# Kernel optimization log

Hardware: AMD Instinct MI355X
Metric: run time of the kernel (lower is better)

The kernel has to match this reference:

```python
import jax, jax.numpy as jnp
import numpy as np

S = 8192          # past KV length
H = 4096          # hidden size
NH = 32           # heads
HD = 128          # head dim
INNER = 16384     # MLP inner (4h)
ROT = 64          # rotary dim per 2D-rope half
NUM_LAYERS = 28
LAYER_ID = 0
ALPHA = (2.0 * NUM_LAYERS) ** 0.5
QK_COEFF = float(LAYER_ID + 1)            # query_key_layer_scaling_coeff
COEFF = (128.0 ** 0.5) * QK_COEFF         # math.sqrt(128) * coeff
EPS = 1e-5


def layernorm(x, w, b):
    mu = jnp.mean(x, axis=-1, keepdims=True)
    var = jnp.var(x, axis=-1, keepdims=True)
    return (x - mu) * jax.lax.rsqrt(var + EPS) * w + b


def rotate_half(x):
    # x: [..., 64]; GLM rotate-half at 32
    return jnp.concatenate([-x[..., 32:], x[..., :32]], axis=-1)


def setup_inputs() -> dict:
    key = jax.random.key(0)
    ks = jax.random.split(key, 16)
    # rotary cache (as in the driver script)
    inv_freq = 1.0 / (10000.0 ** (jnp.arange(0, ROT, 2, dtype=jnp.float32) / ROT))  # [32]
    t = jnp.arange(512, dtype=jnp.float32)
    freqs = jnp.einsum('i,j->ij', t, inv_freq)          # [512,32]
    emb = jnp.concatenate([freqs, freqs], axis=-1)      # [512,64]
    w = lambda k, shp: jax.random.normal(k, shp, dtype=jnp.float32) * 0.02
    return {
        'hidden_states': jax.random.normal(ks[0], (1, H), dtype=jnp.float32),
        'past_key': jax.random.normal(ks[1], (S, NH, HD), dtype=jnp.float32),
        'past_value': jax.random.normal(ks[2], (S, NH, HD), dtype=jnp.float32),
        'cos_cached': jnp.cos(emb),
        'sin_cached': jnp.sin(emb),
        'ln1_w': jnp.ones((H,), jnp.float32), 'ln1_b': jnp.zeros((H,), jnp.float32),
        'qkv_w': w(ks[3], (3 * H, H)), 'qkv_b': w(ks[4], (3 * H,)),
        'dense_w': w(ks[5], (H, H)), 'dense_b': w(ks[6], (H,)),
        'ln2_w': jnp.ones((H,), jnp.float32), 'ln2_b': jnp.zeros((H,), jnp.float32),
        'fc1_w': w(ks[7], (INNER, H)), 'fc1_b': w(ks[8], (INNER,)),
        'fc2_w': w(ks[9], (H, INNER)), 'fc2_b': w(ks[10], (H,)),
        'position_ids': jax.random.randint(ks[11], (1, 1), 0, 512),
        'block_position_ids': jax.random.randint(ks[12], (1, 1), 0, 512),
        'attention_mask': jnp.zeros((1, 1, S + 1), dtype=bool),
    }


def reference(hidden_states, past_key, past_value, cos_cached, sin_cached,
              ln1_w, ln1_b, qkv_w, qkv_b, dense_w, dense_b,
              ln2_w, ln2_b, fc1_w, fc1_b, fc2_w, fc2_b,
              position_ids, block_position_ids, attention_mask):
    # rotary lookups: embedding then transpose(0,1) -> [q_len,1,64]
    pos_cos = jnp.transpose(cos_cached[position_ids], (1, 0, 2))
    pos_sin = jnp.transpose(sin_cached[position_ids], (1, 0, 2))
    blk_cos = jnp.transpose(cos_cached[block_position_ids], (1, 0, 2))
    blk_sin = jnp.transpose(sin_cached[block_position_ids], (1, 0, 2))

    residual = layernorm(hidden_states, ln1_w, ln1_b)          # [1, H]
    qkv = residual @ qkv_w.T + qkv_b                           # [1, 3H]
    qkv = qkv.reshape(-1, NH, 3 * HD)                          # [1, 32, 384]
    query, key_new, value_new = jnp.split(qkv, 3, axis=2)      # each [1,32,128]

    q1, q2 = jnp.split(query, 2, axis=2)                       # [1,32,64] each
    k1, k2 = jnp.split(key_new, 2, axis=2)
    q1 = q1 * pos_cos + rotate_half(q1) * pos_sin
    k1 = k1 * pos_cos + rotate_half(k1) * pos_sin
    q2 = q2 * blk_cos + rotate_half(q2) * blk_sin
    k2 = k2 * blk_cos + rotate_half(k2) * blk_sin
    q = jnp.concatenate([q1, q2], axis=-1)                     # [1,32,128]
    k_new = jnp.concatenate([k1, k2], axis=-1)                 # [1,32,128]

    k = jnp.concatenate([past_key, k_new], axis=0)             # [S+1,32,128]
    v = jnp.concatenate([past_value, value_new], axis=0)       # [S+1,32,128]

    # scores: [heads, q=1, S+1]
    scores = jnp.einsum('qhd,khd->hqk', q / COEFF, k)
    scores = jnp.where(attention_mask, jnp.float32(-10000.0), scores)
    scores = scores * QK_COEFF
    probs = jax.nn.softmax(scores, axis=-1)
    ctx = jnp.einsum('hqk,khd->qhd', probs, v).reshape(-1, H)  # [1,4096]

    attn_out = ctx @ dense_w.T + dense_b
    hidden = residual * ALPHA + attn_out

    residual2 = layernorm(hidden, ln2_w, ln2_b)
    mlp = jax.nn.gelu(residual2 @ fc1_w.T + fc1_b, approximate=True)
    mlp = mlp @ fc2_w.T + fc2_b
    out = residual2 * ALPHA + mlp
    return (out, k, v)
```

## Files before the change

kernel.cpp:

```cpp
#include <hip/hip_runtime.h>
#include <math.h>

#define S_PAST 8192
#define S_TOT  8193
#define HID    4096
#define NH     32
#define HD     128
#define INNER  16384
#define CH     16
#define NCH    512
#define ALPHA_ 7.483314773547883f
#define INV_COEFF 0.08838834764831845f
#define EPS_ 1e-5f

__global__ __launch_bounds__(256) void ln_kernel(const float* __restrict__ xin,
                                                 const float* __restrict__ w,
                                                 const float* __restrict__ b,
                                                 float* __restrict__ out) {
    int tid = threadIdx.x;
    float xs[16];
    float s = 0.f, s2 = 0.f;
#pragma unroll
    for (int i = 0; i < 16; ++i) {
        float v = xin[tid + i * 256];
        xs[i] = v; s += v; s2 += v * v;
    }
    for (int off = 32; off; off >>= 1) {
        s  += __shfl_down(s, off, 64);
        s2 += __shfl_down(s2, off, 64);
    }
    __shared__ float rs[4], rs2[4];
    __shared__ float mu_s, ri_s;
    int wid = tid >> 6, lane = tid & 63;
    if (lane == 0) { rs[wid] = s; rs2[wid] = s2; }
    __syncthreads();
    if (tid == 0) {
        float S1 = rs[0] + rs[1] + rs[2] + rs[3];
        float S2 = rs2[0] + rs2[1] + rs2[2] + rs2[3];
        float mu = S1 / HID;
        float var = S2 / HID - mu * mu;
        mu_s = mu;
        ri_s = rsqrtf(var + EPS_);
    }
    __syncthreads();
    float mu = mu_s, ri = ri_s;
#pragma unroll
    for (int i = 0; i < 16; ++i) {
        int idx = tid + i * 256;
        out[idx] = (xs[i] - mu) * ri * w[idx] + b[idx];
    }
}

template <int C, int MODE>
__global__ __launch_bounds__(256) void gemv_kernel(
        const float* __restrict__ Wm, const float* __restrict__ bias,
        const float* __restrict__ x, float* __restrict__ y,
        const float* __restrict__ res) {
    int wid = threadIdx.x >> 6, lane = threadIdx.x & 63;
    int r = blockIdx.x * 4 + wid;
    const float4* __restrict__ rowv = (const float4*)(Wm + (size_t)r * C);
    const float4* __restrict__ xv = (const float4*)x;
    constexpr int IT = C / 4 / 64;
    float acc0 = 0.f, acc1 = 0.f;
#pragma unroll 8
    for (int it = 0; it < IT; it += 2) {
        float4 w0 = rowv[lane + it * 64];
        float4 x0 = xv[lane + it * 64];
        float4 w1 = rowv[lane + (it + 1) * 64];
        float4 x1 = xv[lane + (it + 1) * 64];
        acc0 += w0.x * x0.x + w0.y * x0.y + w0.z * x0.z + w0.w * x0.w;
        acc1 += w1.x * x1.x + w1.y * x1.y + w1.z * x1.z + w1.w * x1.w;
    }
    float acc = acc0 + acc1;
    for (int off = 32; off; off >>= 1) acc += __shfl_down(acc, off, 64);
    if (lane == 0) {
        float t = acc + bias[r];
        if (MODE == 1) t += ALPHA_ * res[r];
        if (MODE == 2) {
            float u = t;
            t = 0.5f * u * (1.f + tanhf(0.7978845608028654f * (u + 0.044715f * u * u * u)));
        }
        y[r] = t;
    }
}

__global__ __launch_bounds__(128) void rope_kv_kernel(
        const float* __restrict__ qkv, const float* __restrict__ cosc,
        const float* __restrict__ sinc, const int* __restrict__ pos_ids,
        const int* __restrict__ blk_ids, float* __restrict__ qrot,
        float* __restrict__ kout, float* __restrict__ vout) {
    int h = blockIdx.x, d = threadIdx.x;
    int pos = pos_ids[0], blk = blk_ids[0];
    const float* qh = qkv + h * 384;
    float q = qh[d], k = qh[128 + d], v = qh[256 + d];
    int half = d >> 6;
    int i = d & 63;
    int p = half ? blk : pos;
    float c = cosc[p * 64 + i];
    float s = sinc[p * 64 + i];
    float qpart, kpart;
    int base = half * 64;
    if (i < 32) { qpart = -qh[base + i + 32]; kpart = -qh[128 + base + i + 32]; }
    else        { qpart =  qh[base + i - 32]; kpart =  qh[128 + base + i - 32]; }
    float qo = q * c + qpart * s;
    float ko = k * c + kpart * s;
    qrot[h * HD + d] = qo * INV_COEFF;
    size_t o = (size_t)S_PAST * HID + h * HD + d;
    kout[o] = ko;
    vout[o] = v;
}

__global__ __launch_bounds__(512) void attn_onepass(
        const float* __restrict__ qrot, const float* __restrict__ pastk,
        const float* __restrict__ pastv, float* __restrict__ kout,
        float* __restrict__ vout, const unsigned char* __restrict__ mask,
        float* __restrict__ pctx, float* __restrict__ pL) {
    int tid = threadIdx.x;
    int t = tid & 255, u = tid >> 8;
    int s0 = blockIdx.x * CH;
    int rows = (blockIdx.x == NCH - 1) ? (S_TOT - s0) : CH;
    int rstart = u * 8;
    int rend = u ? rows : 8;
    int a = t >> 5;
    const float4* __restrict__ qv = (const float4*)qrot;
    float4 q0 = qv[t], q1 = qv[256 + t], q2 = qv[512 + t], q3 = qv[768 + t];
    float4 a0 = {0,0,0,0}, a1 = {0,0,0,0}, a2 = {0,0,0,0}, a3 = {0,0,0,0};
    float eL0 = 0.f, eL1 = 0.f, eL2 = 0.f, eL3 = 0.f;
#pragma unroll 4
    for (int r = rstart; r < rend; ++r) {
        int srow = s0 + r;
        bool past = srow < S_PAST;
        const float* kbase = past ? pastk : kout;
        const float4* krow = (const float4*)(kbase + (size_t)srow * HID);
        float4 k0 = krow[t], k1 = krow[256 + t];
        float4 k2 = krow[512 + t], k3 = krow[768 + t];
        if (past) {
            float4* ko = (float4*)(kout + (size_t)srow * HID);
            ko[t] = k0; ko[256 + t] = k1; ko[512 + t] = k2; ko[768 + t] = k3;
        }
        float d0 = q0.x * k0.x + q0.y * k0.y + q0.z * k0.z + q0.w * k0.w;
        float d1 = q1.x * k1.x + q1.y * k1.y + q1.z * k1.z + q1.w * k1.w;
        float d2 = q2.x * k2.x + q2.y * k2.y + q2.z * k2.z + q2.w * k2.w;
        float d3 = q3.x * k3.x + q3.y * k3.y + q3.z * k3.z + q3.w * k3.w;
#pragma unroll
        for (int off = 1; off < 32; off <<= 1) {
            d0 += __shfl_xor(d0, off, 64);
            d1 += __shfl_xor(d1, off, 64);
            d2 += __shfl_xor(d2, off, 64);
            d3 += __shfl_xor(d3, off, 64);
        }
        if (mask[srow]) { d0 = d1 = d2 = d3 = -10000.f; }
        float p0 = __expf(d0), p1 = __expf(d1), p2 = __expf(d2), p3 = __expf(d3);
        eL0 += p0; eL1 += p1; eL2 += p2; eL3 += p3;
        const float* vbase = past ? pastv : vout;
        const float4* vrow = (const float4*)(vbase + (size_t)srow * HID);
        float4 v0 = vrow[t], v1 = vrow[256 + t];
        float4 v2 = vrow[512 + t], v3 = vrow[768 + t];
        if (past) {
            float4* vo = (float4*)(vout + (size_t)srow * HID);
            vo[t] = v0; vo[256 + t] = v1; vo[512 + t] = v2; vo[768 + t] = v3;
        }
        a0.x += p0 * v0.x; a0.y += p0 * v0.y; a0.z += p0 * v0.z; a0.w += p0 * v0.w;
        a1.x += p1 * v1.x; a1.y += p1 * v1.y; a1.z += p1 * v1.z; a1.w += p1 * v1.w;
        a2.x += p2 * v2.x; a2.y += p2 * v2.y; a2.z += p2 * v2.z; a2.w += p2 * v2.w;
        a3.x += p3 * v3.x; a3.y += p3 * v3.y; a3.z += p3 * v3.z; a3.w += p3 * v3.w;
    }
    __shared__ float acc_lds[256][16];
    __shared__ float eLds[2][8][4];
    if (u == 1) {
        acc_lds[t][0]  = a0.x; acc_lds[t][1]  = a0.y; acc_lds[t][2]  = a0.z; acc_lds[t][3]  = a0.w;
        acc_lds[t][4]  = a1.x; acc_lds[t][5]  = a1.y; acc_lds[t][6]  = a1.z; acc_lds[t][7]  = a1.w;
        acc_lds[t][8]  = a2.x; acc_lds[t][9]  = a2.y; acc_lds[t][10] = a2.z; acc_lds[t][11] = a2.w;
        acc_lds[t][12] = a3.x; acc_lds[t][13] = a3.y; acc_lds[t][14] = a3.z; acc_lds[t][15] = a3.w;
    }
    if ((t & 31) == 0) {
        eLds[u][a][0] = eL0; eLds[u][a][1] = eL1;
        eLds[u][a][2] = eL2; eLds[u][a][3] = eL3;
    }
    __syncthreads();
    if (u == 0) {
        a0.x += acc_lds[t][0];  a0.y += acc_lds[t][1];  a0.z += acc_lds[t][2];  a0.w += acc_lds[t][3];
        a1.x += acc_lds[t][4];  a1.y += acc_lds[t][5];  a1.z += acc_lds[t][6];  a1.w += acc_lds[t][7];
        a2.x += acc_lds[t][8];  a2.y += acc_lds[t][9];  a2.z += acc_lds[t][10]; a2.w += acc_lds[t][11];
        a3.x += acc_lds[t][12]; a3.y += acc_lds[t][13]; a3.z += acc_lds[t][14]; a3.w += acc_lds[t][15];
        float4* pc = (float4*)(pctx + (size_t)blockIdx.x * HID);
        pc[t] = a0; pc[256 + t] = a1; pc[512 + t] = a2; pc[768 + t] = a3;
    }
    if (tid < NH) {
        int ah = tid & 7, g = tid >> 3;
        pL[tid * NCH + blockIdx.x] = eLds[0][ah][g] + eLds[1][ah][g];
    }
}

__global__ __launch_bounds__(256) void ctx_reduce1(const float* __restrict__ pctx,
                                                   const float* __restrict__ pL,
                                                   float* __restrict__ pctx2,
                                                   float* __restrict__ pL2) {
    int b = blockIdx.x, tid = threadIdx.x;
    float4 a0 = {0,0,0,0}, a1 = {0,0,0,0}, a2 = {0,0,0,0}, a3 = {0,0,0,0};
#pragma unroll
    for (int c = 0; c < 8; ++c) {
        const float4* row = (const float4*)(pctx + (size_t)(b * 8 + c) * HID);
        float4 v0 = row[tid], v1 = row[256 + tid], v2 = row[512 + tid], v3 = row[768 + tid];
        a0.x += v0.x; a0.y += v0.y; a0.z += v0.z; a0.w += v0.w;
        a1.x += v1.x; a1.y += v1.y; a1.z += v1.z; a1.w += v1.w;
        a2.x += v2.x; a2.y += v2.y; a2.z += v2.z; a2.w += v2.w;
        a3.x += v3.x; a3.y += v3.y; a3.z += v3.z; a3.w += v3.w;
    }
    float4* o = (float4*)(pctx2 + (size_t)b * HID);
    o[tid] = a0; o[256 + tid] = a1; o[512 + tid] = a2; o[768 + tid] = a3;
    if (tid < NH) {
        float s = 0.f;
#pragma unroll
        for (int c = 0; c < 8; ++c) s += pL[tid * NCH + b * 8 + c];
        pL2[tid * 64 + b] = s;
    }
}

__global__ __launch_bounds__(256) void ctx_reduce2(const float* __restrict__ pctx2,
                                                   const float* __restrict__ pL2,
                                                   float* __restrict__ ctx) {
    int tid = threadIdx.x;
    __shared__ float Lh[NH];
    if (tid < NH) {
        float s = 0.f;
        for (int j = 0; j < 64; ++j) s += pL2[tid * 64 + j];
        Lh[tid] = s;
    }
    __syncthreads();
    int idx = blockIdx.x * 256 + tid;
    float a = 0.f;
    for (int c = 0; c < 64; ++c) a += pctx2[(size_t)c * HID + idx];
    ctx[idx] = a / Lh[idx >> 7];
}

extern "C" void kernel_launch(void* const* d_in, const int* in_sizes, int n_in,
                              void* d_out, int out_size, void* d_ws, size_t ws_size,
                              hipStream_t stream) {
    const float* hidden = (const float*)d_in[0];
    const float* past_k = (const float*)d_in[1];
    const float* past_v = (const float*)d_in[2];
    const float* cosc = (const float*)d_in[3];
    const float* sinc = (const float*)d_in[4];
    const float* ln1w = (const float*)d_in[5];
    const float* ln1b = (const float*)d_in[6];
    const float* qkvw = (const float*)d_in[7];
    const float* qkvb = (const float*)d_in[8];
    const float* denw = (const float*)d_in[9];
    const float* denb = (const float*)d_in[10];
    const float* ln2w = (const float*)d_in[11];
    const float* ln2b = (const float*)d_in[12];
    const float* fc1w = (const float*)d_in[13];
    const float* fc1b = (const float*)d_in[14];
    const float* fc2w = (const float*)d_in[15];
    const float* fc2b = (const float*)d_in[16];
    const int* pos = (const int*)d_in[17];
    const int* blk = (const int*)d_in[18];
    const unsigned char* mask = (const unsigned char*)d_in[19];

    float* out_f = (float*)d_out;
    float* kout = out_f + HID;
    float* vout = kout + (size_t)S_TOT * HID;

    float* ws = (float*)d_ws;
    float* resid1 = ws;
    float* qkvv   = ws + 4096;
    float* qrot   = ws + 16384;
    float* ctx    = ws + 20480;
    float* hid2   = ws + 24576;
    float* resid2 = ws + 28672;
    float* mlpi   = ws + 32768;
    float* pL     = ws + 49152;
    float* pL2    = ws + 65536;
    float* pctx   = ws + 67584;
    float* pctx2  = ws + 2164736;

    ln_kernel<<<1, 256, 0, stream>>>(hidden, ln1w, ln1b, resid1);
    gemv_kernel<HID, 0><<<3 * HID / 4, 256, 0, stream>>>(qkvw, qkvb, resid1, qkvv, nullptr);
    rope_kv_kernel<<<NH, HD, 0, stream>>>(qkvv, cosc, sinc, pos, blk, qrot, kout, vout);
    attn_onepass<<<NCH, 512, 0, stream>>>(qrot, past_k, past_v, kout, vout, mask, pctx, pL);
    ctx_reduce1<<<64, 256, 0, stream>>>(pctx, pL, pctx2, pL2);
    ctx_reduce2<<<16, 256, 0, stream>>>(pctx2, pL2, ctx);
    gemv_kernel<HID, 1><<<HID / 4, 256, 0, stream>>>(denw, denb, ctx, hid2, resid1);
    ln_kernel<<<1, 256, 0, stream>>>(hid2, ln2w, ln2b, resid2);
    gemv_kernel<HID, 2><<<INNER / 4, 256, 0, stream>>>(fc1w, fc1b, resid2, mlpi, nullptr);
    gemv_kernel<INNER, 1><<<HID / 4, 256, 0, stream>>>(fc2w, fc2b, mlpi, out_f, resid2);
}
```

Before: 288.2 us.

## Split KV-cache copy into dedicated nontemporal kernel and merge ctx reductions

Moves the past K/V copy out of the attention loop into a separate grid-stride kernel that uses nontemporal loads and stores. Attention now only reads K/V. The two-stage context reduction is also folded into one 256-block kernel that sums all 512 partials per column slice directly. The cost is that past K/V is now read twice from HBM (once by the copy, once by attention) instead of once, in exchange for simpler attention stores and one fewer launch.

```diff
diff --git a/kernel.cpp b/kernel.cpp
--- a/kernel.cpp
+++ b/kernel.cpp
@@ -12,6 +12,8 @@
 #define ALPHA_ 7.483314773547883f
 #define INV_COEFF 0.08838834764831845f
 #define EPS_ 1e-5f
+
+typedef float vf4 __attribute__((ext_vector_type(4)));
 
 __global__ __launch_bounds__(256) void ln_kernel(const float* __restrict__ xin,
                                                  const float* __restrict__ w,
@@ -110,10 +112,26 @@
     vout[o] = v;
 }
 
+#define COPY_GRID 2048
+__global__ __launch_bounds__(256) void kv_copy(const vf4* __restrict__ pk,
+                                               const vf4* __restrict__ pv,
+                                               vf4* __restrict__ ko,
+                                               vf4* __restrict__ vo) {
+    const size_t n = (size_t)S_PAST * HID / 4;
+    int half = blockIdx.x >= (COPY_GRID / 2);
+    const vf4* __restrict__ src = half ? pv : pk;
+    vf4* __restrict__ dst = half ? vo : ko;
+    size_t start = (size_t)(blockIdx.x - half * (COPY_GRID / 2)) * 256 + threadIdx.x;
+    size_t stride = (size_t)(COPY_GRID / 2) * 256;
+    for (size_t i = start; i < n; i += stride) {
+        __builtin_nontemporal_store(__builtin_nontemporal_load(src + i), dst + i);
+    }
+}
+
 __global__ __launch_bounds__(512) void attn_onepass(
         const float* __restrict__ qrot, const float* __restrict__ pastk,
-        const float* __restrict__ pastv, float* __restrict__ kout,
-        float* __restrict__ vout, const unsigned char* __restrict__ mask,
+        const float* __restrict__ pastv, const float* __restrict__ kout,
+        const float* __restrict__ vout, const unsigned char* __restrict__ mask,
         float* __restrict__ pctx, float* __restrict__ pL) {
     int tid = threadIdx.x;
     int t = tid & 255, u = tid >> 8;
@@ -134,10 +152,6 @@
         const float4* krow = (const float4*)(kbase + (size_t)srow * HID);
         float4 k0 = krow[t], k1 = krow[256 + t];
         float4 k2 = krow[512 + t], k3 = krow[768 + t];
-        if (past) {
-            float4* ko = (float4*)(kout + (size_t)srow * HID);
-            ko[t] = k0; ko[256 + t] = k1; ko[512 + t] = k2; ko[768 + t] = k3;
-        }
         float d0 = q0.x * k0.x + q0.y * k0.y + q0.z * k0.z + q0.w * k0.w;
         float d1 = q1.x * k1.x + q1.y * k1.y + q1.z * k1.z + q1.w * k1.w;
         float d2 = q2.x * k2.x + q2.y * k2.y + q2.z * k2.z + q2.w * k2.w;
@@ -156,10 +170,6 @@
         const float4* vrow = (const float4*)(vbase + (size_t)srow * HID);
         float4 v0 = vrow[t], v1 = vrow[256 + t];
         float4 v2 = vrow[512 + t], v3 = vrow[768 + t];
-        if (past) {
-            float4* vo = (float4*)(vout + (size_t)srow * HID);
-            vo[t] = v0; vo[256 + t] = v1; vo[512 + t] = v2; vo[768 + t] = v3;
-        }
         a0.x += p0 * v0.x; a0.y += p0 * v0.y; a0.z += p0 * v0.z; a0.w += p0 * v0.w;
         a1.x += p1 * v1.x; a1.y += p1 * v1.y; a1.z += p1 * v1.z; a1.w += p1 * v1.w;
         a2.x += p2 * v2.x; a2.y += p2 * v2.y; a2.z += p2 * v2.z; a2.w += p2 * v2.w;
@@ -192,46 +202,30 @@
     }
 }
 
-__global__ __launch_bounds__(256) void ctx_reduce1(const float* __restrict__ pctx,
-                                                   const float* __restrict__ pL,
-                                                   float* __restrict__ pctx2,
-                                                   float* __restrict__ pL2) {
-    int b = blockIdx.x, tid = threadIdx.x;
-    float4 a0 = {0,0,0,0}, a1 = {0,0,0,0}, a2 = {0,0,0,0}, a3 = {0,0,0,0};
-#pragma unroll
-    for (int c = 0; c < 8; ++c) {
-        const float4* row = (const float4*)(pctx + (size_t)(b * 8 + c) * HID);
-        float4 v0 = row[tid], v1 = row[256 + tid], v2 = row[512 + tid], v3 = row[768 + tid];
-        a0.x += v0.x; a0.y += v0.y; a0.z += v0.z; a0.w += v0.w;
-        a1.x += v1.x; a1.y += v1.y; a1.z += v1.z; a1.w += v1.w;
-        a2.x += v2.x; a2.y += v2.y; a2.z += v2.z; a2.w += v2.w;
-        a3.x += v3.x; a3.y += v3.y; a3.z += v3.z; a3.w += v3.w;
-    }
-    float4* o = (float4*)(pctx2 + (size_t)b * HID);
-    o[tid] = a0; o[256 + tid] = a1; o[512 + tid] = a2; o[768 + tid] = a3;
-    if (tid < NH) {
+__global__ __launch_bounds__(256) void ctx_reduce(const float* __restrict__ pctx,
+                                                  const float* __restrict__ pL,
+                                                  float* __restrict__ ctx) {
+    int b = blockIdx.x, t = threadIdx.x;
+    int i0 = b * 16;
+    int h = i0 >> 7;
+    float e = pL[h * NCH + t] + pL[h * NCH + 256 + t];
+    for (int off = 32; off; off >>= 1) e += __shfl_down(e, off, 64);
+    __shared__ float ew[4];
+    int wid = t >> 6, lane = t & 63;
+    if (lane == 0) ew[wid] = e;
+    int r0 = t >> 4, ii = t & 15;
+    float a = 0.f;
+    for (int r = r0; r < NCH; r += 16) a += pctx[(size_t)r * HID + i0 + ii];
+    __shared__ float sc[16][17];
+    sc[r0][ii] = a;
+    __syncthreads();
+    float Lh = ew[0] + ew[1] + ew[2] + ew[3];
+    if (t < 16) {
         float s = 0.f;
 #pragma unroll
-        for (int c = 0; c < 8; ++c) s += pL[tid * NCH + b * 8 + c];
-        pL2[tid * 64 + b] = s;
-    }
-}
-
-__global__ __launch_bounds__(256) void ctx_reduce2(const float* __restrict__ pctx2,
-                                                   const float* __restrict__ pL2,
-                                                   float* __restrict__ ctx) {
-    int tid = threadIdx.x;
-    __shared__ float Lh[NH];
-    if (tid < NH) {
-        float s = 0.f;
-        for (int j = 0; j < 64; ++j) s += pL2[tid * 64 + j];
-        Lh[tid] = s;
-    }
-    __syncthreads();
-    int idx = blockIdx.x * 256 + tid;
-    float a = 0.f;
-    for (int c = 0; c < 64; ++c) a += pctx2[(size_t)c * HID + idx];
-    ctx[idx] = a / Lh[idx >> 7];
+        for (int r = 0; r < 16; ++r) s += sc[r][t];
+        ctx[i0 + t] = s / Lh;
+    }
 }
 
 extern "C" void kernel_launch(void* const* d_in, const int* in_sizes, int n_in,
@@ -271,16 +265,15 @@
     float* resid2 = ws + 28672;
     float* mlpi   = ws + 32768;
     float* pL     = ws + 49152;
-    float* pL2    = ws + 65536;
-    float* pctx   = ws + 67584;
-    float* pctx2  = ws + 2164736;
+    float* pctx   = ws + 65536;
 
     ln_kernel<<<1, 256, 0, stream>>>(hidden, ln1w, ln1b, resid1);
     gemv_kernel<HID, 0><<<3 * HID / 4, 256, 0, stream>>>(qkvw, qkvb, resid1, qkvv, nullptr);
     rope_kv_kernel<<<NH, HD, 0, stream>>>(qkvv, cosc, sinc, pos, blk, qrot, kout, vout);
+    kv_copy<<<COPY_GRID, 256, 0, stream>>>((const vf4*)past_k, (const vf4*)past_v,
+                                           (vf4*)kout, (vf4*)vout);
     attn_onepass<<<NCH, 512, 0, stream>>>(qrot, past_k, past_v, kout, vout, mask, pctx, pL);
-    ctx_reduce1<<<64, 256, 0, stream>>>(pctx, pL, pctx2, pL2);
-    ctx_reduce2<<<16, 256, 0, stream>>>(pctx2, pL2, ctx);
+    ctx_reduce<<<256, 256, 0, stream>>>(pctx, pL, ctx);
     gemv_kernel<HID, 1><<<HID / 4, 256, 0, stream>>>(denw, denb, ctx, hid2, resid1);
     ln_kernel<<<1, 256, 0, stream>>>(hid2, ln2w, ln2b, resid2);
     gemv_kernel<HID, 2><<<INNER / 4, 256, 0, stream>>>(fc1w, fc1b, resid2, mlpi, nullptr);
```

After: 312.7 us. 1.08x slower.
